# Optimization experiments

Hardware: AMD Instinct MI355X
Metric: run time of the kernel (lower is better)

The kernel has to match this reference:

```python
import jax, jax.numpy as jnp
import numpy as np

VOCAB = 50257
HIDDEN = 2048
BATCH = 8
SEQ = 2048
TOPK = 256


def setup_inputs() -> dict:
    key = jax.random.key(0)
    k1, k2 = jax.random.split(key)
    input_ids = jax.random.randint(k1, (BATCH, SEQ), 0, VOCAB, dtype=jnp.int64)
    W = jax.random.normal(k2, (VOCAB, HIDDEN), dtype=jnp.float32)
    return {"input_ids": input_ids, "W": W, "k": TOPK}


def reference(input_ids, W, k):
    # Embedding gather: [B, S] ids -> [B, S, H] logits (irregular row gather).
    logits = jnp.take(W, input_ids, axis=0)
    # Top-k over the last (hidden) dim, sorted descending (matches torch.topk).
    values, indices = jax.lax.top_k(logits, k)
    return values, indices.astype(jnp.int32)
```

## Files before the change

kernel.cpp:

```cpp
#include <hip/hip_runtime.h>
#include <stdint.h>

#define VOCAB  50257
#define HIDDEN 2048
#define NTOK   (8 * 2048)
#define TOPK   256

__global__ __launch_bounds__(256) void topk_kernel(
    const int* __restrict__ ids,
    const float* __restrict__ W,
    float* __restrict__ out)
{
    const int t   = threadIdx.x;
    const int row = blockIdx.x;

    __shared__ uint32_t hist[256];
    __shared__ uint32_t scan[256];
    __shared__ uint64_t sel[256];
    __shared__ uint32_t s_digit, s_rem, s_all, s_cnt;

    const int id = ids[row];
    const float4* src = reinterpret_cast<const float4*>(W + (size_t)id * HIDDEN);
    float4 a = src[t];
    float4 b = src[t + 256];

    float vals[8] = {a.x, a.y, a.z, a.w, b.x, b.y, b.z, b.w};
    uint64_t key[8];
#pragma unroll
    for (int e = 0; e < 8; ++e) {
        uint32_t u = __float_as_uint(vals[e]);
        u = (u & 0x80000000u) ? ~u : (u | 0x80000000u);
        int idx = (e < 4) ? (4 * t + e) : (1024 + 4 * t + (e - 4));
        key[e] = ((uint64_t)u << 16) | (uint32_t)((~idx) & 0xFFFF);
    }

    uint64_t prefix = 0;
    uint32_t rem    = TOPK;
    uint64_t T      = 0;

    for (int bp = 40; bp >= 0; bp -= 8) {
        hist[t] = 0;
        __syncthreads();
#pragma unroll
        for (int e = 0; e < 8; ++e) {
            if ((key[e] >> (bp + 8)) == prefix)
                atomicAdd(&hist[(uint32_t)(key[e] >> bp) & 0xFFu], 1u);
        }
        __syncthreads();
        scan[t] = hist[t];
        __syncthreads();
        for (int off = 1; off < 256; off <<= 1) {
            uint32_t add = (t + off < 256) ? scan[t + off] : 0u;
            __syncthreads();
            scan[t] += add;
            __syncthreads();
        }
        uint32_t ge = scan[t];
        uint32_t gt = (t == 255) ? 0u : scan[t + 1];
        if (ge >= rem && gt < rem) {
            s_digit = (uint32_t)t;
            s_rem   = rem - gt;
            s_all   = ((rem - gt) == hist[t]) ? 1u : 0u;
        }
        __syncthreads();
        prefix = (prefix << 8) | s_digit;
        rem    = s_rem;
        uint32_t all = s_all;
        __syncthreads();
        if (all || bp == 0) {
            T = prefix << bp;
            break;
        }
    }

    if (t == 0) s_cnt = 0;
    __syncthreads();
#pragma unroll
    for (int e = 0; e < 8; ++e) {
        if (key[e] >= T) {
            uint32_t p = atomicAdd(&s_cnt, 1u);
            if (p < 256u) sel[p] = key[e];
        }
    }
    __syncthreads();

    for (int k2 = 2; k2 <= 256; k2 <<= 1) {
        for (int j = k2 >> 1; j > 0; j >>= 1) {
            int ixj = t ^ j;
            if (ixj > t) {
                uint64_t x = sel[t], y = sel[ixj];
                bool desc = ((t & k2) == 0);
                bool sw = desc ? (x < y) : (x > y);
                if (sw) { sel[t] = y; sel[ixj] = x; }
            }
            __syncthreads();
        }
    }

    uint64_t kk = sel[t];
    uint32_t s  = (uint32_t)(kk >> 16);
    uint32_t u  = (s & 0x80000000u) ? (s & 0x7FFFFFFFu) : ~s;
    int idx     = (int)((~(uint32_t)kk) & 0xFFFF);

    out[(size_t)row * TOPK + t] = __uint_as_float(u);
    out[(size_t)NTOK * TOPK + (size_t)row * TOPK + t] = (float)idx;
}

extern "C" void kernel_launch(void* const* d_in, const int* in_sizes, int n_in,
                              void* d_out, int out_size, void* d_ws, size_t ws_size,
                              hipStream_t stream) {
    const int*   ids = (const int*)d_in[0];
    const float* W   = (const float*)d_in[1];
    float* out = (float*)d_out;

    topk_kernel<<<NTOK, 256, 0, stream>>>(ids, W, out);
}
```

Baseline: 595.8 us.

## Process one row per wavefront with shuffle-based radix select and bitonic sort

Each 64-lane wavefront now handles a whole row (32 values per lane), so a block of 256 threads processes four rows. The radix-select histogram scan uses wave shuffles plus an active-element mask, and the bitonic sort keeps 4 keys per lane in registers and exchanges them via shuffles. All block-wide __syncthreads are gone. The cost is higher register pressure (32 values per lane) and reliance on wavefront-synchronous LDS behaviour with only __threadfence_block for ordering.

```diff
diff --git a/kernel.cpp b/kernel.cpp
--- a/kernel.cpp
+++ b/kernel.cpp
@@ -5,105 +5,195 @@
 #define HIDDEN 2048
 #define NTOK   (8 * 2048)
 #define TOPK   256
+#define WPB    4
+
+
+__device__ __forceinline__ void cmpex(uint64_t& a, uint64_t& b, bool desc) {
+    bool gt = a > b;
+    uint64_t mx = gt ? a : b;
+    uint64_t mn = gt ? b : a;
+    a = desc ? mx : mn;
+    b = desc ? mn : mx;
+}
+
+__device__ __forceinline__ void step_xor(uint64_t& v, int r, int lane, int lx, int k) {
+    uint64_t p = __shfl_xor(v, lx, 64);
+    int i = lane * 4 + r;
+    bool desc = ((i & k) == 0);
+    bool low  = ((lane & lx) == 0);
+    bool keep_max = (desc == low);
+    bool gt = v > p;
+    v = (keep_max == gt) ? v : p;
+}
 
 __global__ __launch_bounds__(256) void topk_kernel(
     const int* __restrict__ ids,
     const float* __restrict__ W,
     float* __restrict__ out)
 {
-    const int t   = threadIdx.x;
-    const int row = blockIdx.x;
-
-    __shared__ uint32_t hist[256];
-    __shared__ uint32_t scan[256];
-    __shared__ uint64_t sel[256];
-    __shared__ uint32_t s_digit, s_rem, s_all, s_cnt;
+    const int lane = threadIdx.x & 63;
+    const int w    = threadIdx.x >> 6;
+    const int row  = blockIdx.x * WPB + w;
+
+    __shared__ uint32_t hist[WPB][256];
+    __shared__ __align__(16) uint64_t sel[WPB][256];
+    __shared__ uint32_t cnt[WPB];
 
     const int id = ids[row];
-    const float4* src = reinterpret_cast<const float4*>(W + (size_t)id * HIDDEN);
-    float4 a = src[t];
-    float4 b = src[t + 256];
-
-    float vals[8] = {a.x, a.y, a.z, a.w, b.x, b.y, b.z, b.w};
-    uint64_t key[8];
-#pragma unroll
-    for (int e = 0; e < 8; ++e) {
-        uint32_t u = __float_as_uint(vals[e]);
-        u = (u & 0x80000000u) ? ~u : (u | 0x80000000u);
-        int idx = (e < 4) ? (4 * t + e) : (1024 + 4 * t + (e - 4));
-        key[e] = ((uint64_t)u << 16) | (uint32_t)((~idx) & 0xFFFF);
-    }
-
+    const float4* src = (const float4*)(W + (size_t)id * HIDDEN);
+
+    uint32_t sv[32];
+#pragma unroll
+    for (int c = 0; c < 8; ++c) {
+        float4 v = src[c * 64 + lane];
+        uint32_t u[4] = {__float_as_uint(v.x), __float_as_uint(v.y),
+                         __float_as_uint(v.z), __float_as_uint(v.w)};
+#pragma unroll
+        for (int j = 0; j < 4; ++j) {
+            uint32_t m = (u[j] & 0x80000000u) ? 0xFFFFFFFFu : 0x80000000u;
+            sv[c * 4 + j] = u[j] ^ m;
+        }
+    }
+
+    uint32_t active = 0xFFFFFFFFu;
+    uint32_t rem    = TOPK;
     uint64_t prefix = 0;
-    uint32_t rem    = TOPK;
-    uint64_t T      = 0;
-
+    uint64_t Tkey   = 0;
+    bool done = false;
+
+#pragma unroll
     for (int bp = 40; bp >= 0; bp -= 8) {
-        hist[t] = 0;
-        __syncthreads();
-#pragma unroll
-        for (int e = 0; e < 8; ++e) {
-            if ((key[e] >> (bp + 8)) == prefix)
-                atomicAdd(&hist[(uint32_t)(key[e] >> bp) & 0xFFu], 1u);
-        }
-        __syncthreads();
-        scan[t] = hist[t];
-        __syncthreads();
-        for (int off = 1; off < 256; off <<= 1) {
-            uint32_t add = (t + off < 256) ? scan[t + off] : 0u;
-            __syncthreads();
-            scan[t] += add;
-            __syncthreads();
-        }
-        uint32_t ge = scan[t];
-        uint32_t gt = (t == 255) ? 0u : scan[t + 1];
-        if (ge >= rem && gt < rem) {
-            s_digit = (uint32_t)t;
-            s_rem   = rem - gt;
-            s_all   = ((rem - gt) == hist[t]) ? 1u : 0u;
-        }
-        __syncthreads();
-        prefix = (prefix << 8) | s_digit;
-        rem    = s_rem;
-        uint32_t all = s_all;
-        __syncthreads();
-        if (all || bp == 0) {
-            T = prefix << bp;
-            break;
-        }
-    }
-
-    if (t == 0) s_cnt = 0;
-    __syncthreads();
-#pragma unroll
-    for (int e = 0; e < 8; ++e) {
-        if (key[e] >= T) {
-            uint32_t p = atomicAdd(&s_cnt, 1u);
-            if (p < 256u) sel[p] = key[e];
-        }
-    }
-    __syncthreads();
-
-    for (int k2 = 2; k2 <= 256; k2 <<= 1) {
-        for (int j = k2 >> 1; j > 0; j >>= 1) {
-            int ixj = t ^ j;
-            if (ixj > t) {
-                uint64_t x = sel[t], y = sel[ixj];
-                bool desc = ((t & k2) == 0);
-                bool sw = desc ? (x < y) : (x > y);
-                if (sw) { sel[t] = y; sel[ixj] = x; }
-            }
-            __syncthreads();
-        }
-    }
-
-    uint64_t kk = sel[t];
-    uint32_t s  = (uint32_t)(kk >> 16);
-    uint32_t u  = (s & 0x80000000u) ? (s & 0x7FFFFFFFu) : ~s;
-    int idx     = (int)((~(uint32_t)kk) & 0xFFFF);
-
-    out[(size_t)row * TOPK + t] = __uint_as_float(u);
-    out[(size_t)NTOK * TOPK + (size_t)row * TOPK + t] = (float)idx;
+        if (!done) {
+            *(uint4*)&hist[w][lane * 4] = make_uint4(0u, 0u, 0u, 0u);
+            __threadfence_block();
+#pragma unroll
+            for (int e = 0; e < 32; ++e) {
+                if (active & (1u << e)) {
+                    uint32_t d;
+                    if (bp >= 16) {
+                        d = (sv[e] >> (bp - 16)) & 0xFFu;
+                    } else {
+                        uint32_t idx = (uint32_t)((e >> 2) * 256 + lane * 4 + (e & 3));
+                        d = ((0xFFFFu ^ idx) >> bp) & 0xFFu;
+                    }
+                    atomicAdd(&hist[w][d], 1u);
+                }
+            }
+            __threadfence_block();
+
+            uint4 h = *(uint4*)&hist[w][lane * 4];
+            uint32_t s3 = h.w;
+            uint32_t s2 = h.z + s3;
+            uint32_t s1 = h.y + s2;
+            uint32_t s0 = h.x + s1;
+            uint32_t suf = s0;
+#pragma unroll
+            for (int off = 1; off < 64; off <<= 1) {
+                uint32_t t2 = __shfl_down(suf, off, 64);
+                suf += (lane + off < 64) ? t2 : 0u;
+            }
+            uint32_t above = suf - s0;
+
+            uint32_t dsel = 0, grp = 0, nrem = 0;
+            bool found = false;
+            uint32_t hm[4] = {h.x, h.y, h.z, h.w};
+            uint32_t sm[4] = {s0, s1, s2, s3};
+#pragma unroll
+            for (int m = 0; m < 4; ++m) {
+                uint32_t ge = above + sm[m];
+                uint32_t gt = ge - hm[m];
+                if (ge >= rem && gt < rem) {
+                    found = true;
+                    dsel = (uint32_t)(lane * 4 + m);
+                    grp  = hm[m];
+                    nrem = rem - gt;
+                }
+            }
+            uint64_t ball = __ballot(found);
+            int srcl = __builtin_ctzll(ball);
+            uint64_t pack = ((uint64_t)dsel << 32) | ((uint64_t)grp << 16) | nrem;
+            pack = __shfl(pack, srcl, 64);
+            dsel = (uint32_t)(pack >> 32);
+            grp  = (uint32_t)((pack >> 16) & 0xFFFFu);
+            nrem = (uint32_t)(pack & 0xFFFFu);
+
+            prefix = (prefix << 8) | dsel;
+            rem = nrem;
+            if (grp == nrem) {
+                Tkey = prefix << bp;
+                done = true;
+            } else {
+#pragma unroll
+                for (int e = 0; e < 32; ++e) {
+                    if (active & (1u << e)) {
+                        uint32_t d;
+                        if (bp >= 16) {
+                            d = (sv[e] >> (bp - 16)) & 0xFFu;
+                        } else {
+                            uint32_t idx = (uint32_t)((e >> 2) * 256 + lane * 4 + (e & 3));
+                            d = ((0xFFFFu ^ idx) >> bp) & 0xFFu;
+                        }
+                        if (d != dsel) active &= ~(1u << e);
+                    }
+                }
+            }
+        }
+    }
+
+    if (lane == 0) cnt[w] = 0;
+    __threadfence_block();
+#pragma unroll
+    for (int e = 0; e < 32; ++e) {
+        uint32_t idx = (uint32_t)((e >> 2) * 256 + lane * 4 + (e & 3));
+        uint64_t kk = ((uint64_t)sv[e] << 16) | (uint64_t)(0xFFFFu ^ idx);
+        if (kk >= Tkey) {
+            uint32_t p = atomicAdd(&cnt[w], 1u);
+            if (p < 256u) sel[w][p] = kk;
+        }
+    }
+    __threadfence_block();
+
+    uint64_t v0 = sel[w][lane * 4 + 0];
+    uint64_t v1 = sel[w][lane * 4 + 1];
+    uint64_t v2 = sel[w][lane * 4 + 2];
+    uint64_t v3 = sel[w][lane * 4 + 3];
+
+#pragma unroll
+    for (int k = 2; k <= 256; k <<= 1) {
+#pragma unroll
+        for (int j = 128; j >= 4; j >>= 1) {
+            if (j <= (k >> 1)) {
+                int lx = j >> 2;
+                step_xor(v0, 0, lane, lx, k);
+                step_xor(v1, 1, lane, lx, k);
+                step_xor(v2, 2, lane, lx, k);
+                step_xor(v3, 3, lane, lx, k);
+            }
+        }
+        if (k >= 4) {
+            bool d02 = (((lane * 4 + 0) & k) == 0);
+            bool d13 = (((lane * 4 + 1) & k) == 0);
+            cmpex(v0, v2, d02);
+            cmpex(v1, v3, d13);
+        }
+        bool d01 = (((lane * 4 + 0) & k) == 0);
+        bool d23 = (((lane * 4 + 2) & k) == 0);
+        cmpex(v0, v1, d01);
+        cmpex(v2, v3, d23);
+    }
+
+    uint64_t kk[4] = {v0, v1, v2, v3};
+    float ov[4], oi[4];
+#pragma unroll
+    for (int r = 0; r < 4; ++r) {
+        uint32_t s = (uint32_t)(kk[r] >> 16);
+        ov[r] = __uint_as_float((s & 0x80000000u) ? (s & 0x7FFFFFFFu) : ~s);
+        oi[r] = (float)(0xFFFFu ^ (uint32_t)(kk[r] & 0xFFFFu));
+    }
+    float4* out_v = (float4*)(out + (size_t)row * TOPK);
+    float4* out_i = (float4*)(out + (size_t)NTOK * TOPK + (size_t)row * TOPK);
+    out_v[lane] = make_float4(ov[0], ov[1], ov[2], ov[3]);
+    out_i[lane] = make_float4(oi[0], oi[1], oi[2], oi[3]);
 }
 
 extern "C" void kernel_launch(void* const* d_in, const int* in_sizes, int n_in,
@@ -113,5 +203,5 @@
     const float* W   = (const float*)d_in[1];
     float* out = (float*)d_out;
 
-    topk_kernel<<<NTOK, 256, 0, stream>>>(ids, W, out);
-}
+    topk_kernel<<<NTOK / WPB, 256, 0, stream>>>(ids, W, out);
+}
```

Result: faster. 535.0 us (-10.2%).
